# Kernel optimization log

Measured on AMD Instinct MI355X. Metric: run time of the kernel, lower is better.

## Reference

```python
import jax, jax.numpy as jnp
import numpy as np

DIM = 1024
NUM_HEADS = 16
HEAD_DIM = DIM // NUM_HEADS


def setup_inputs() -> dict:
    key = jax.random.key(0)
    k_x, k_wqkv, k_bqkv, k_wo, k_bo = jax.random.split(key, 5)
    B, N = 2, 2048
    s = 1.0 / np.sqrt(DIM)
    return {
        "x": jax.random.normal(k_x, (B, N, DIM), dtype=jnp.float32),
        "w_qkv": jax.random.uniform(k_wqkv, (DIM, 3 * DIM), jnp.float32, -s, s),
        "b_qkv": jax.random.uniform(k_bqkv, (3 * DIM,), jnp.float32, -s, s),
        "w_out": jax.random.uniform(k_wo, (DIM, DIM), jnp.float32, -s, s),
        "b_out": jax.random.uniform(k_bo, (DIM,), jnp.float32, -s, s),
    }


def reference(x, w_qkv, b_qkv, w_out, b_out):
    B, N, D = x.shape
    H, Hd = NUM_HEADS, HEAD_DIM
    scale = Hd ** -0.5
    qkv = x @ w_qkv + b_qkv                      # [B,N,3D]
    qkv = qkv.reshape(B, N, 3, H, Hd).transpose(2, 0, 3, 1, 4)  # [3,B,H,N,Hd]
    q, k, v = qkv[0], qkv[1], qkv[2]
    scores = jnp.einsum("bhqd,bhkd->bhqk", q, k) * scale
    attn = jax.nn.softmax(scores, axis=-1)
    out = jnp.einsum("bhqk,bhkd->bhqd", attn, v)  # [B,H,N,Hd]
    out = out.transpose(0, 2, 1, 3).reshape(B, N, D)
    return out @ w_out + b_out
```

## Files before the change

### kernel.cpp

```cpp
#include <hip/hip_runtime.h>
#include <stdint.h>

#define D_MODEL 1024
#define NHEADS 16
#define HDIM 64
#define BATCH 2
#define SEQ 2048
#define MTOK (BATCH*SEQ)

typedef unsigned short u16;
typedef __attribute__((ext_vector_type(8))) __bf16 bf16x8;
typedef __attribute__((ext_vector_type(8))) unsigned short u16x8;
typedef __attribute__((ext_vector_type(4))) unsigned short u16x4;
typedef __attribute__((ext_vector_type(4))) float f32x4;
typedef __attribute__((ext_vector_type(16))) float f32x16;
typedef __attribute__((ext_vector_type(2))) unsigned int u32x2;

__device__ __forceinline__ u16 f2bf(float f) {
  union { float f; uint32_t u; } v; v.f = f;
  uint32_t u = v.u;
  u += 0x7fffu + ((u >> 16) & 1u);
  return (u16)(u >> 16);
}

__device__ __forceinline__ unsigned cvtpk(float a, float b) {
  unsigned r;
  asm("v_cvt_pk_bf16_f32 %0, %1, %2" : "=v"(r) : "v"(a), "v"(b));
  return r;
}

__device__ __forceinline__ u32x2 plswap(unsigned a, unsigned b) {
#if __has_builtin(__builtin_amdgcn_permlane32_swap)
  return __builtin_amdgcn_permlane32_swap(a, b, false, false);
#else
  asm("v_permlane32_swap_b32 %0, %1" : "+v"(a), "+v"(b));
  u32x2 r; r.x = a; r.y = b; return r;
#endif
}

__device__ __forceinline__ void async16(u16* lds, const u16* g) {
  __builtin_amdgcn_global_load_lds(
      (__attribute__((address_space(1))) void*)(u16*)g,
      (__attribute__((address_space(3))) void*)lds,
      16, 0, 0);
}

__device__ __forceinline__ void transpose_cast_body(
    const float* __restrict__ in, u16* __restrict__ out, int R, int C,
    int bid, int tid, float (*tile)[33])
{
  int nCB = C >> 5;
  int bc = bid % nCB, br = bid / nCB;
  int r0 = br * 32, c0 = bc * 32;
  int tx = tid & 31, ty = tid >> 5;
#pragma unroll
  for (int i = 0; i < 4; ++i)
    tile[ty + i*8][tx] = in[(size_t)(r0 + ty + i*8) * C + c0 + tx];
  __syncthreads();
#pragma unroll
  for (int i = 0; i < 4; ++i)
    out[(size_t)(c0 + ty + i*8) * R + r0 + tx] = f2bf(tile[tx][ty + i*8]);
}

__global__ __launch_bounds__(256) void prep_kernel(
    const float* __restrict__ x, const float* __restrict__ w_qkv,
    const float* __restrict__ w_out,
    u16* __restrict__ x_bf, u16* __restrict__ wqkv_t, u16* __restrict__ wout_t)
{
  __shared__ float tile[32][33];
  int bid = blockIdx.x, tid = threadIdx.x;
  if (bid < 2048) {
    int i = bid * 256 + tid;
    const float4* p = (const float4*)(x + (size_t)i * 8);
    float4 a = p[0], b = p[1];
    u16x8 r;
    r[0]=f2bf(a.x); r[1]=f2bf(a.y); r[2]=f2bf(a.z); r[3]=f2bf(a.w);
    r[4]=f2bf(b.x); r[5]=f2bf(b.y); r[6]=f2bf(b.z); r[7]=f2bf(b.w);
    *(u16x8*)(x_bf + (size_t)i * 8) = r;
  } else if (bid < 2048 + 3072) {
    transpose_cast_body(w_qkv, wqkv_t, 1024, 3072, bid - 2048, tid, tile);
  } else {
    transpose_cast_body(w_out, wout_t, 1024, 1024, bid - 5120, tid, tile);
  }
}

__global__ __launch_bounds__(512, 6) void gemm_qkv_kernel(
    const u16* __restrict__ A, const u16* __restrict__ Bt,
    const float* __restrict__ bias,
    u16* __restrict__ qb, u16* __restrict__ kb, u16* __restrict__ vt,
    int M, int Nn, int K)
{
  __shared__ alignas(16) u16 As[128 * 64];
  __shared__ alignas(16) u16 Bs[128 * 64];

  const int tid = threadIdx.x;
  const int wid = tid >> 6, lane = tid & 63;
  const int col = lane & 15, kg = lane >> 4;
  const int csw = (col & 7) << 3;

  const int nTN = Nn >> 7;
  int bidx = blockIdx.x;
  {
    int cpx = gridDim.x >> 3;
    bidx = (bidx & 7) * cpx + (bidx >> 3);
  }
  const int tile_m = (bidx / nTN) << 7;
  const int tile_n = (bidx % nTN) << 7;
  const int wm = (wid >> 2) << 6;
  const int wn = (wid & 3) << 5;

  f32x4 acc[4][2] = {};

  const int sr = tid >> 3;
  const int sc = (tid & 7) << 3;
  const int ssc = sc ^ ((sr & 7) << 3);

  const int nk = K >> 6;
  for (int kt = 0; kt < nk; ++kt) {
    __syncthreads();
#pragma unroll
    for (int i = 0; i < 2; ++i)
      async16(&As[(i*64 + sr) * 64 + sc],
              A + (size_t)(tile_m + i*64 + sr) * K + kt*64 + ssc);
#pragma unroll
    for (int i = 0; i < 2; ++i)
      async16(&Bs[(i*64 + sr) * 64 + sc],
              Bt + (size_t)(tile_n + i*64 + sr) * K + kt*64 + ssc);
    __syncthreads();

#pragma unroll
    for (int ks = 0; ks < 2; ++ks) {
      bf16x8 af[4], bfv[2];
#pragma unroll
      for (int i = 0; i < 4; ++i)
        af[i] = *(const bf16x8*)&As[(wm + i*16 + col) * 64 + ((ks*32 + kg*8) ^ csw)];
#pragma unroll
      for (int j = 0; j < 2; ++j)
        bfv[j] = *(const bf16x8*)&Bs[(wn + j*16 + col) * 64 + ((ks*32 + kg*8) ^ csw)];
#pragma unroll
      for (int i = 0; i < 4; ++i)
#pragma unroll
        for (int j = 0; j < 2; ++j)
          acc[i][j] = __builtin_amdgcn_mfma_f32_16x16x32_bf16(af[i], bfv[j], acc[i][j], 0, 0, 0);
    }
  }

#pragma unroll
  for (int i = 0; i < 4; ++i) {
#pragma unroll
    for (int jn = 0; jn < 2; ++jn) {
      const int gcol = tile_n + wn + jn*16 + col;
      const float bv = bias[gcol];
      const int grow0 = tile_m + wm + i*16 + kg*4;
      const int btok = grow0 >> 11, tok0 = grow0 & 2047;
      const int which = gcol >> 10, f = gcol & 1023;
      const int h = f >> 6, hd = f & 63;
      if (which == 2) {
        u16x4 pk;
#pragma unroll
        for (int j = 0; j < 4; ++j) pk[j] = f2bf(acc[i][jn][j] + bv);
        *(u16x4*)&vt[((size_t)(btok*NHEADS + h) * HDIM + hd) * SEQ + tok0] = pk;
      } else {
#pragma unroll
        for (int j = 0; j < 4; ++j) {
          float val = acc[i][jn][j] + bv;
          size_t dst = ((size_t)(btok*NHEADS + h) * SEQ + tok0 + j) * HDIM + hd;
          if (which == 0) qb[dst] = f2bf(val * 0.18033688f);
          else            kb[dst] = f2bf(val);
        }
      }
    }
  }
}

__global__ __launch_bounds__(512, 4) void gemm_out_kernel(
    const u16* __restrict__ A, const u16* __restrict__ Bt,
    const float* __restrict__ bias, float* __restrict__ outF,
    int M, int Nn, int K)
{
  __shared__ alignas(16) u16 As[64 * 64];
  __shared__ alignas(16) u16 Bs[128 * 64];

  const int tid = threadIdx.x;
  const int wid = tid >> 6, lane = tid & 63;
  const int col = lane & 15, kg = lane >> 4;
  const int csw = (col & 7) << 3;

  const int nTN = Nn >> 7;
  int bidx = blockIdx.x;
  {
    int cpx = gridDim.x >> 3;
    bidx = (bidx & 7) * cpx + (bidx >> 3);
  }
  const int tile_m = (bidx / nTN) << 6;
  const int tile_n = (bidx % nTN) << 7;
  const int wn = wid << 4;

  f32x4 acc[4] = {};

  const int sr = tid >> 3;
  const int sc = (tid & 7) << 3;
  const int ssc = sc ^ ((sr & 7) << 3);

  const int nk = K >> 6;
  for (int kt = 0; kt < nk; ++kt) {
    __syncthreads();
    async16(&As[sr * 64 + sc],
            A + (size_t)(tile_m + sr) * K + kt*64 + ssc);
#pragma unroll
    for (int i = 0; i < 2; ++i)
      async16(&Bs[(i*64 + sr) * 64 + sc],
              Bt + (size_t)(tile_n + i*64 + sr) * K + kt*64 + ssc);
    __syncthreads();

#pragma unroll
    for (int ks = 0; ks < 2; ++ks) {
      bf16x8 bfv = *(const bf16x8*)&Bs[(wn + col) * 64 + ((ks*32 + kg*8) ^ csw)];
#pragma unroll
      for (int i = 0; i < 4; ++i) {
        bf16x8 af = *(const bf16x8*)&As[(i*16 + col) * 64 + ((ks*32 + kg*8) ^ csw)];
        acc[i] = __builtin_amdgcn_mfma_f32_16x16x32_bf16(af, bfv, acc[i], 0, 0, 0);
      }
    }
  }

  const int gcol = tile_n + wn + col;
  const float bv = bias[gcol];
#pragma unroll
  for (int i = 0; i < 4; ++i) {
    const int grow0 = tile_m + i*16 + kg*4;
#pragma unroll
    for (int j = 0; j < 4; ++j)
      outF[(size_t)(grow0 + j) * Nn + gcol] = acc[i][j] + bv;
  }
}

__global__ __launch_bounds__(512, 2) void attn_kernel(
    const u16* __restrict__ qb, const u16* __restrict__ kb,
    const u16* __restrict__ vt, u16* __restrict__ ao)
{
  __shared__ alignas(16) u16 Ks[2][128 * 64];
  __shared__ alignas(16) u16 Vs[2][64 * 128];

  const int tid = threadIdx.x, wid = tid >> 6, lane = tid & 63;
  const int c31 = lane & 31, hi = lane >> 5;
  const int rsw = (lane & 7) << 3;

  int bidx = blockIdx.x;
  bidx = (bidx & 7) * 32 + (bidx >> 3);
  const int bh = bidx >> 3;
  const int qt = bidx & 7;

  const u16* Qh = qb + (size_t)bh * SEQ * HDIM;
  const u16* Kh = kb + (size_t)bh * SEQ * HDIM;
  const u16* Vh = vt + (size_t)bh * SEQ * HDIM;

  const int q0 = qt * 256 + wid * 32;
  bf16x8 qf[4];
#pragma unroll
  for (int kk = 0; kk < 4; ++kk)
    qf[kk] = *(const bf16x8*)(Qh + (size_t)(q0 + c31) * HDIM + kk*16 + hi*8);

  float l_run = 0.f;
  f32x16 o[2] = {};

  const int krow = tid >> 2, kc = (tid & 3) << 4, ksw = (krow & 7) << 3;
  const int vrow = tid >> 3, vc = (tid & 7) << 4, vsw = (vrow & 7) << 3;

  u16x8 kreg[2], vreg[2];
#define LOAD_TILES(t)                                                               \
  {                                                                                 \
    _Pragma("unroll")                                                               \
    for (int i = 0; i < 2; ++i)                                                     \
      kreg[i] = *(const u16x8*)(Kh + (size_t)((t)*128 + krow) * HDIM + kc + i*8);   \
    _Pragma("unroll")                                                               \
    for (int i = 0; i < 2; ++i)                                                     \
      vreg[i] = *(const u16x8*)(Vh + (size_t)vrow * SEQ + (t)*128 + vc + i*8);      \
  }
#define STORE_TILES(b)                                                              \
  {                                                                                 \
    _Pragma("unroll")                                                               \
    for (int i = 0; i < 2; ++i)                                                     \
      *(u16x8*)&Ks[b][krow * 64 + ((kc + i*8) ^ ksw)] = kreg[i];                    \
    _Pragma("unroll")                                                               \
    for (int i = 0; i < 2; ++i)                                                     \
      *(u16x8*)&Vs[b][vrow * 128 + ((vc + i*8) ^ vsw)] = vreg[i];                   \
  }

  LOAD_TILES(0);
  STORE_TILES(0);
  __syncthreads();

  for (int t = 0; t < 16; ++t) {
    const int cur = t & 1;
    if (t < 15) LOAD_TILES(t + 1);

    f32x16 s[4] = {};
#pragma unroll
    for (int kk = 0; kk < 4; ++kk) {
#pragma unroll
      for (int nt = 0; nt < 4; ++nt) {
        bf16x8 kf = *(const bf16x8*)&Ks[cur][(nt*32 + c31) * 64 + ((kk*16 + hi*8) ^ rsw)];
        s[nt] = __builtin_amdgcn_mfma_f32_32x32x16_bf16(kf, qf[kk], s[nt], 0, 0, 0);
      }
    }

#pragma unroll
    for (int nt = 0; nt < 4; ++nt) {
      float sum = 0.f;
#pragma unroll
      for (int r = 0; r < 16; ++r) {
        s[nt][r] = __builtin_amdgcn_exp2f(s[nt][r]);
        sum += s[nt][r];
      }
      l_run += sum;
    }

#pragma unroll
    for (int kk = 0; kk < 8; ++kk) {
      const int nt = kk >> 1, rb = (kk & 1) * 8;
      unsigned A0 = cvtpk(s[nt][rb+0], s[nt][rb+1]);
      unsigned A1 = cvtpk(s[nt][rb+2], s[nt][rb+3]);
      unsigned B0 = cvtpk(s[nt][rb+4], s[nt][rb+5]);
      unsigned B1 = cvtpk(s[nt][rb+6], s[nt][rb+7]);
      u32x2 p0 = plswap(A0, B0);
      u32x2 p1 = plswap(A1, B1);
      union { unsigned w[4]; bf16x8 v; } pf;
      pf.w[0] = p0.x; pf.w[1] = p1.x; pf.w[2] = p0.y; pf.w[3] = p1.y;
#pragma unroll
      for (int dt = 0; dt < 2; ++dt) {
        bf16x8 vf = *(const bf16x8*)&Vs[cur][(dt*32 + c31) * 128 + ((kk*16 + hi*8) ^ rsw)];
        o[dt] = __builtin_amdgcn_mfma_f32_32x32x16_bf16(vf, pf.v, o[dt], 0, 0, 0);
      }
    }

    if (t < 15) {
      STORE_TILES(cur ^ 1);
      __syncthreads();
    }
  }

  const int bb = bh >> 4, h = bh & 15;
  {
    float l = l_run + __shfl_xor(l_run, 32);
    float inv = 1.0f / l;
    const int nrow = q0 + c31;
#pragma unroll
    for (int dt = 0; dt < 2; ++dt) {
#pragma unroll
      for (int tq = 0; tq < 4; ++tq) {
        u16x4 pk;
#pragma unroll
        for (int j = 0; j < 4; ++j) pk[j] = f2bf(o[dt][tq*4 + j] * inv);
        int feat = h*64 + dt*32 + tq*8 + hi*4;
        *(u16x4*)&ao[(size_t)(bb * SEQ + nrow) * D_MODEL + feat] = pk;
      }
    }
  }
#undef LOAD_TILES
#undef STORE_TILES
}

extern "C" void kernel_launch(void* const* d_in, const int* in_sizes, int n_in,
                              void* d_out, int out_size, void* d_ws, size_t ws_size,
                              hipStream_t stream)
{
  const float* x     = (const float*)d_in[0];
  const float* w_qkv = (const float*)d_in[1];
  const float* b_qkv = (const float*)d_in[2];
  const float* w_out = (const float*)d_in[3];
  const float* b_out = (const float*)d_in[4];
  float* out = (float*)d_out;
  (void)in_sizes; (void)n_in; (void)out_size; (void)ws_size;

  char* ws = (char*)d_ws;
  u16* x_bf   = (u16*)(ws);
  u16* wqkv_t = (u16*)(ws + (size_t)( 8 << 20));
  u16* wout_t = (u16*)(ws + (size_t)(14 << 20));
  u16* qb     = (u16*)(ws + (size_t)(16 << 20));
  u16* kb     = (u16*)(ws + (size_t)(24 << 20));
  u16* vt     = (u16*)(ws + (size_t)(32 << 20));
  u16* ao     = (u16*)(ws + (size_t)(40 << 20));

  prep_kernel<<<2048 + 3072 + 1024, 256, 0, stream>>>(x, w_qkv, w_out, x_bf, wqkv_t, wout_t);

  gemm_qkv_kernel<<<(MTOK/128)*(3072/128), 512, 0, stream>>>(
      x_bf, wqkv_t, b_qkv, qb, kb, vt, MTOK, 3072, 1024);

  attn_kernel<<<32*8, 512, 0, stream>>>(qb, kb, vt, ao);

  gemm_out_kernel<<<(MTOK/64)*(1024/128), 512, 0, stream>>>(
      ao, wout_t, b_out, out, MTOK, 1024, 1024);
}
```

Before: 102.7 us.

## Software-pipeline attention loop: overlap next-tile QK with current softmax/PV, triple-buffer LDS

Restructures the attention inner loop so that the QK^T MFMAs for key tile t+1 run alongside the exp/pack and PV MFMAs for tile t. Two score register sets ping-pong, and K/V shared-memory buffers go from double to triple buffering. The aim is to hide the dependency between score computation, softmax and the PV matmul, and to keep the MFMA pipe busier. In exchange, per-block LDS rises to 96KB and score registers double. That likely breaks the 2-blocks-per-CU target in launch_bounds and may cause register pressure or spills.

```diff
diff --git a/kernel.cpp b/kernel.cpp
--- a/kernel.cpp
+++ b/kernel.cpp
@@ -239,8 +239,8 @@
     const u16* __restrict__ qb, const u16* __restrict__ kb,
     const u16* __restrict__ vt, u16* __restrict__ ao)
 {
-  __shared__ alignas(16) u16 Ks[2][128 * 64];
-  __shared__ alignas(16) u16 Vs[2][64 * 128];
+  __shared__ alignas(16) u16 Ks[3][128 * 64];
+  __shared__ alignas(16) u16 Vs[3][64 * 128];
 
   const int tid = threadIdx.x, wid = tid >> 6, lane = tid & 63;
   const int c31 = lane & 31, hi = lane >> 5;
@@ -263,6 +263,7 @@
 
   float l_run = 0.f;
   f32x16 o[2] = {};
+  f32x16 sA[4], sB[4];
 
   const int krow = tid >> 2, kc = (tid & 3) << 4, ksw = (krow & 7) << 3;
   const int vrow = tid >> 3, vc = (tid & 7) << 4, vsw = (vrow & 7) << 3;
@@ -286,59 +287,79 @@
     for (int i = 0; i < 2; ++i)                                                     \
       *(u16x8*)&Vs[b][vrow * 128 + ((vc + i*8) ^ vsw)] = vreg[i];                   \
   }
+#define QK_STEP(SDST, kbuf)                                                         \
+  {                                                                                 \
+    const u16* kbp = (kbuf);                                                        \
+    _Pragma("unroll")                                                               \
+    for (int nt = 0; nt < 4; ++nt)                                                  \
+      _Pragma("unroll")                                                             \
+      for (int r = 0; r < 16; ++r) SDST[nt][r] = 0.f;                               \
+    _Pragma("unroll")                                                               \
+    for (int kk = 0; kk < 4; ++kk) {                                                \
+      _Pragma("unroll")                                                             \
+      for (int nt = 0; nt < 4; ++nt) {                                              \
+        bf16x8 kf = *(const bf16x8*)&kbp[(nt*32 + c31) * 64 + ((kk*16 + hi*8) ^ rsw)]; \
+        SDST[nt] = __builtin_amdgcn_mfma_f32_32x32x16_bf16(kf, qf[kk], SDST[nt], 0, 0, 0); \
+      }                                                                             \
+    }                                                                               \
+  }
+#define FINISH_STEP(SSRC, vbuf)                                                     \
+  {                                                                                 \
+    const u16* vbp = (vbuf);                                                        \
+    _Pragma("unroll")                                                               \
+    for (int nt = 0; nt < 4; ++nt) {                                                \
+      float sum = 0.f;                                                              \
+      _Pragma("unroll")                                                             \
+      for (int r = 0; r < 16; ++r) {                                                \
+        SSRC[nt][r] = __builtin_amdgcn_exp2f(SSRC[nt][r]);                          \
+        sum += SSRC[nt][r];                                                         \
+      }                                                                             \
+      l_run += sum;                                                                 \
+    }                                                                               \
+    _Pragma("unroll")                                                               \
+    for (int kk = 0; kk < 8; ++kk) {                                                \
+      const int nt = kk >> 1, rb = (kk & 1) * 8;                                    \
+      unsigned A0 = cvtpk(SSRC[nt][rb+0], SSRC[nt][rb+1]);                          \
+      unsigned A1 = cvtpk(SSRC[nt][rb+2], SSRC[nt][rb+3]);                          \
+      unsigned B0 = cvtpk(SSRC[nt][rb+4], SSRC[nt][rb+5]);                          \
+      unsigned B1 = cvtpk(SSRC[nt][rb+6], SSRC[nt][rb+7]);                          \
+      u32x2 p0 = plswap(A0, B0);                                                    \
+      u32x2 p1 = plswap(A1, B1);                                                    \
+      union { unsigned w[4]; bf16x8 v; } pf;                                        \
+      pf.w[0] = p0.x; pf.w[1] = p1.x; pf.w[2] = p0.y; pf.w[3] = p1.y;               \
+      _Pragma("unroll")                                                             \
+      for (int dt = 0; dt < 2; ++dt) {                                              \
+        bf16x8 vf = *(const bf16x8*)&vbp[(dt*32 + c31) * 128 + ((kk*16 + hi*8) ^ rsw)]; \
+        o[dt] = __builtin_amdgcn_mfma_f32_32x32x16_bf16(vf, pf.v, o[dt], 0, 0, 0);  \
+      }                                                                             \
+    }                                                                               \
+  }
 
   LOAD_TILES(0);
   STORE_TILES(0);
   __syncthreads();
-
-  for (int t = 0; t < 16; ++t) {
-    const int cur = t & 1;
-    if (t < 15) LOAD_TILES(t + 1);
-
-    f32x16 s[4] = {};
-#pragma unroll
-    for (int kk = 0; kk < 4; ++kk) {
-#pragma unroll
-      for (int nt = 0; nt < 4; ++nt) {
-        bf16x8 kf = *(const bf16x8*)&Ks[cur][(nt*32 + c31) * 64 + ((kk*16 + hi*8) ^ rsw)];
-        s[nt] = __builtin_amdgcn_mfma_f32_32x32x16_bf16(kf, qf[kk], s[nt], 0, 0, 0);
-      }
-    }
-
-#pragma unroll
-    for (int nt = 0; nt < 4; ++nt) {
-      float sum = 0.f;
-#pragma unroll
-      for (int r = 0; r < 16; ++r) {
-        s[nt][r] = __builtin_amdgcn_exp2f(s[nt][r]);
-        sum += s[nt][r];
-      }
-      l_run += sum;
-    }
-
-#pragma unroll
-    for (int kk = 0; kk < 8; ++kk) {
-      const int nt = kk >> 1, rb = (kk & 1) * 8;
-      unsigned A0 = cvtpk(s[nt][rb+0], s[nt][rb+1]);
-      unsigned A1 = cvtpk(s[nt][rb+2], s[nt][rb+3]);
-      unsigned B0 = cvtpk(s[nt][rb+4], s[nt][rb+5]);
-      unsigned B1 = cvtpk(s[nt][rb+6], s[nt][rb+7]);
-      u32x2 p0 = plswap(A0, B0);
-      u32x2 p1 = plswap(A1, B1);
-      union { unsigned w[4]; bf16x8 v; } pf;
-      pf.w[0] = p0.x; pf.w[1] = p1.x; pf.w[2] = p0.y; pf.w[3] = p1.y;
-#pragma unroll
-      for (int dt = 0; dt < 2; ++dt) {
-        bf16x8 vf = *(const bf16x8*)&Vs[cur][(dt*32 + c31) * 128 + ((kk*16 + hi*8) ^ rsw)];
-        o[dt] = __builtin_amdgcn_mfma_f32_32x32x16_bf16(vf, pf.v, o[dt], 0, 0, 0);
-      }
-    }
-
-    if (t < 15) {
-      STORE_TILES(cur ^ 1);
-      __syncthreads();
-    }
-  }
+  QK_STEP(sA, Ks[0]);
+  LOAD_TILES(1);
+  STORE_TILES(1);
+  __syncthreads();
+
+  for (int k = 0; k < 7; ++k) {
+    const int t1 = 2*k + 1;
+    LOAD_TILES(t1 + 1);
+    QK_STEP(sB, Ks[t1 % 3]);
+    FINISH_STEP(sA, Vs[(t1 - 1) % 3]);
+    STORE_TILES((t1 + 1) % 3);
+    __syncthreads();
+    const int t2 = t1 + 1;
+    LOAD_TILES(t2 + 1);
+    QK_STEP(sA, Ks[t2 % 3]);
+    FINISH_STEP(sB, Vs[(t2 - 1) % 3]);
+    STORE_TILES((t2 + 1) % 3);
+    __syncthreads();
+  }
+  QK_STEP(sB, Ks[0]);
+  FINISH_STEP(sA, Vs[2]);
+  FINISH_STEP(sB, Vs[0]);
 
   const int bb = bh >> 4, h = bh & 15;
   {
@@ -359,6 +380,8 @@
   }
 #undef LOAD_TILES
 #undef STORE_TILES
+#undef QK_STEP
+#undef FINISH_STEP
 }
 
 extern "C" void kernel_launch(void* const* d_in, const int* in_sizes, int n_in,
```

Result: slower. 110.0 us (+7.1%).
